# Optimization experiments

Measured on AMD Instinct MI355X. Metric: run time of the kernel, lower is better.

The kernel has to match this reference:

```python
import jax, jax.numpy as jnp
import numpy as np

T_STEPS, BATCH, DH, L = 256, 128, 512, 3  # L=3 is the only shape-consistent conv length (kernel=3, no pad)


def _conv3(x, W, b):
    # Conv1d(Dh->2, k=3) on a length-3 signal == full contraction over (Dh, 3)
    # x: (B, Dh, 3), W: (2, Dh, 3), b: (2,) -> (B, 2, 1)
    out = jnp.einsum('bdl,odl->bo', x, W) + b
    return out[:, :, None]


def setup_inputs() -> dict:
    key = jax.random.key(0)
    ks = jax.random.split(key, 5)
    inputs = jax.random.normal(ks[0], (T_STEPS, BATCH, DH, L), dtype=jnp.float32)
    h0 = jnp.zeros((BATCH, DH, L), jnp.float32)
    c0 = jnp.zeros((BATCH, DH, L), jnp.float32)
    scale = 1.0 / np.sqrt(DH * L).astype(np.float32)
    Wr = jax.random.normal(ks[1], (2, DH, L), jnp.float32) * scale  # recurrent_kernel (orthogonal-ish init)
    br = jnp.full((2,), 0.5, jnp.float32)                           # recurrent bias init 0.5
    Wc = jax.random.normal(ks[2], (2, DH, L), jnp.float32) * scale  # cell_memory_kernel
    bc = jnp.zeros((2,), jnp.float32)                               # cell_memory bias init 0
    Wi = jax.random.normal(ks[3], (2, DH, L), jnp.float32) * scale  # input_kernel
    bi = jax.random.normal(ks[4], (2,), jnp.float32) * scale
    return dict(inputs=inputs, h0=h0, c0=c0, Wr=Wr, br=br, Wc=Wc, bc=bc, Wi=Wi, bi=bi)


def reference(inputs, h0, c0, Wr, br, Wc, bc, Wi, bi):
    sig = jax.nn.sigmoid  # fun_gate

    def step(state, xt):
        h, c = state  # (B, Dh, 3) each
        cm = _conv3(c, Wc, bc)
        Cc, Ch = cm[:, 0:1], cm[:, 1:2]   # (B,1,1) each (chunk(2, dim=1))
        rm = _conv3(h, Wr, br)
        Hc, Hh = rm[:, 0:1], rm[:, 1:2]
        im = _conv3(xt, Wi, bi)
        Xc, Xh = im[:, 0:1], im[:, 1:2]
        gh = (1.0 - sig(Ch)) * Xh + (1.0 - sig(Hh)) * h   # broadcast (B,1,1)*(B,Dh,3)
        gc = (1.0 - sig(Hc)) * Xc + (1.0 - sig(Cc)) * c
        ht = jnp.tanh(gh)  # fun_main
        ct = jnp.tanh(gc)
        return (ht, ct), ht

    (hT, cT), outs = jax.lax.scan(step, (h0, c0), inputs)
    return outs, hT, cT
```

## Files before the change

### kernel.cpp

```cpp
#include <hip/hip_runtime.h>

#define T_STEPS 256
#define BATCH   128
#define FEAT    1536
#define NPAIRS  (T_STEPS * BATCH)

template <int CTRL, int RMASK>
__device__ __forceinline__ float dpp_add_step(float v) {
    int m = __builtin_amdgcn_update_dpp(0, __float_as_int(v), CTRL, RMASK, 0xF, true);
    return v + __int_as_float(m);
}

__device__ __forceinline__ float wave_reduce63(float v) {
    v = dpp_add_step<0x111, 0xF>(v);
    v = dpp_add_step<0x112, 0xF>(v);
    v = dpp_add_step<0x114, 0xF>(v);
    v = dpp_add_step<0x118, 0xF>(v);
    v = dpp_add_step<0x142, 0xA>(v);
    v = dpp_add_step<0x143, 0xC>(v);
    return v;
}

__device__ __forceinline__ float one_minus_sig(float x) {
    float e = __builtin_amdgcn_exp2f(x * 1.4426950408889634f);
    return __builtin_amdgcn_rcpf(1.0f + e);
}

__device__ __forceinline__ float tanh_fast(float x) {
    float e = __builtin_amdgcn_exp2f(x * 2.8853900817779268f);
    return fmaf(-2.0f, __builtin_amdgcn_rcpf(1.0f + e), 1.0f);
}

__device__ __forceinline__ void barrier_lds_only() {
    asm volatile("s_waitcnt lgkmcnt(0)\n\ts_barrier" ::: "memory");
}

__global__ __launch_bounds__(256) void scan_fused_kernel(
    const float* __restrict__ inputs,
    const float* __restrict__ h0,
    const float* __restrict__ c0,
    const float* __restrict__ Wr, const float* __restrict__ br,
    const float* __restrict__ Wc, const float* __restrict__ bc,
    const float* __restrict__ Wi, const float* __restrict__ bi,
    float* __restrict__ outs,
    float* __restrict__ hT,
    float* __restrict__ cT)
{
    const int b    = blockIdx.x;
    const int tid  = threadIdx.x;
    const int wid  = tid >> 6;
    const int lane = tid & 63;

    __shared__ float4 red4[2][4];
    __shared__ float2 red2[2][4];

    const float4 wr0_4 = ((const float4*)Wr)[tid];
    const float4 wr1_4 = ((const float4*)(Wr + FEAT))[tid];
    const float2 wr0_2 = ((const float2*)(Wr + 1024))[tid];
    const float2 wr1_2 = ((const float2*)(Wr + FEAT + 1024))[tid];
    const float4 wc0_4 = ((const float4*)Wc)[tid];
    const float4 wc1_4 = ((const float4*)(Wc + FEAT))[tid];
    const float2 wc0_2 = ((const float2*)(Wc + 1024))[tid];
    const float2 wc1_2 = ((const float2*)(Wc + FEAT + 1024))[tid];
    const float4 wi0_4 = ((const float4*)Wi)[tid];
    const float4 wi1_4 = ((const float4*)(Wi + FEAT))[tid];
    const float2 wi0_2 = ((const float2*)(Wi + 1024))[tid];
    const float2 wi1_2 = ((const float2*)(Wi + FEAT + 1024))[tid];
    const float br0 = br[0], br1 = br[1];
    const float bc0 = bc[0], bc1 = bc[1];
    const float bi0 = bi[0], bi1 = bi[1];

    const float* h0b = h0 + (size_t)b * FEAT;
    const float* c0b = c0 + (size_t)b * FEAT;
    float4 h4 = ((const float4*)h0b)[tid];
    float2 h2 = ((const float2*)(h0b + 1024))[tid];
    float4 c4 = ((const float4*)c0b)[tid];
    float2 c2 = ((const float2*)(c0b + 1024))[tid];

    const float*  xbase   = inputs + (size_t)b * FEAT;
    const size_t  XSTRIDE = (size_t)BATCH * FEAT;

    float4 xa4 = ((const float4*)xbase)[tid];
    float2 xa2 = ((const float2*)(xbase + 1024))[tid];
    float4 xb4 = ((const float4*)(xbase + XSTRIDE))[tid];
    float2 xb2 = ((const float2*)(xbase + XSTRIDE + 1024))[tid];

    float* op = outs + (size_t)b * FEAT;
    const size_t OSTRIDE = (size_t)BATCH * FEAT;

    auto step = [&](float4* buf4, float2* buf2, int t, float4& x4, float2& x2) {
        float pHc = h4.x * wr0_4.x + h4.y * wr0_4.y + h4.z * wr0_4.z + h4.w * wr0_4.w
                  + h2.x * wr0_2.x + h2.y * wr0_2.y;
        float pHh = h4.x * wr1_4.x + h4.y * wr1_4.y + h4.z * wr1_4.z + h4.w * wr1_4.w
                  + h2.x * wr1_2.x + h2.y * wr1_2.y;
        float pCc = c4.x * wc0_4.x + c4.y * wc0_4.y + c4.z * wc0_4.z + c4.w * wc0_4.w
                  + c2.x * wc0_2.x + c2.y * wc0_2.y;
        float pCh = c4.x * wc1_4.x + c4.y * wc1_4.y + c4.z * wc1_4.z + c4.w * wc1_4.w
                  + c2.x * wc1_2.x + c2.y * wc1_2.y;
        float pXc = x4.x * wi0_4.x + x4.y * wi0_4.y + x4.z * wi0_4.z + x4.w * wi0_4.w
                  + x2.x * wi0_2.x + x2.y * wi0_2.y;
        float pXh = x4.x * wi1_4.x + x4.y * wi1_4.y + x4.z * wi1_4.z + x4.w * wi1_4.w
                  + x2.x * wi1_2.x + x2.y * wi1_2.y;

        {
            const int tn = (t + 2 < T_STEPS) ? (t + 2) : (T_STEPS - 1);
            const float* xp = xbase + (size_t)tn * XSTRIDE;
            x4 = ((const float4*)xp)[tid];
            x2 = ((const float2*)(xp + 1024))[tid];
        }

        pHc = wave_reduce63(pHc);
        pHh = wave_reduce63(pHh);
        pCc = wave_reduce63(pCc);
        pCh = wave_reduce63(pCh);
        pXc = wave_reduce63(pXc);
        pXh = wave_reduce63(pXh);

        if (lane == 63) {
            buf4[wid] = make_float4(pHc, pHh, pCc, pCh);
            buf2[wid] = make_float2(pXc, pXh);
        }
        barrier_lds_only();
        const float4 r0 = buf4[0];
        const float4 r1 = buf4[1];
        const float4 r2 = buf4[2];
        const float4 r3 = buf4[3];
        const float2 s0 = buf2[0];
        const float2 s1 = buf2[1];
        const float2 s2 = buf2[2];
        const float2 s3 = buf2[3];
        const float Hc = r0.x + r1.x + r2.x + r3.x + br0;
        const float Hh = r0.y + r1.y + r2.y + r3.y + br1;
        const float Cc = r0.z + r1.z + r2.z + r3.z + bc0;
        const float Ch = r0.w + r1.w + r2.w + r3.w + bc1;
        const float Xc = s0.x + s1.x + s2.x + s3.x + bi0;
        const float Xh = s0.y + s1.y + s2.y + s3.y + bi1;

        const float Ah = one_minus_sig(Ch) * Xh;
        const float Sh = one_minus_sig(Hh);
        const float Ac = one_minus_sig(Hc) * Xc;
        const float Sc = one_minus_sig(Cc);

        h4.x = tanh_fast(fmaf(Sh, h4.x, Ah));
        h4.y = tanh_fast(fmaf(Sh, h4.y, Ah));
        h4.z = tanh_fast(fmaf(Sh, h4.z, Ah));
        h4.w = tanh_fast(fmaf(Sh, h4.w, Ah));
        h2.x = tanh_fast(fmaf(Sh, h2.x, Ah));
        h2.y = tanh_fast(fmaf(Sh, h2.y, Ah));

        c4.x = tanh_fast(fmaf(Sc, c4.x, Ac));
        c4.y = tanh_fast(fmaf(Sc, c4.y, Ac));
        c4.z = tanh_fast(fmaf(Sc, c4.z, Ac));
        c4.w = tanh_fast(fmaf(Sc, c4.w, Ac));
        c2.x = tanh_fast(fmaf(Sc, c2.x, Ac));
        c2.y = tanh_fast(fmaf(Sc, c2.y, Ac));

        ((float4*)op)[tid]          = h4;
        ((float2*)(op + 1024))[tid] = h2;
        op += OSTRIDE;
    };

#pragma unroll 1
    for (int t = 0; t < T_STEPS; t += 2) {
        step(red4[0], red2[0], t,     xa4, xa2);
        step(red4[1], red2[1], t + 1, xb4, xb2);
    }

    float* hp = hT + (size_t)b * FEAT;
    ((float4*)hp)[tid]          = h4;
    ((float2*)(hp + 1024))[tid] = h2;
    float* cp = cT + (size_t)b * FEAT;
    ((float4*)cp)[tid]          = c4;
    ((float2*)(cp + 1024))[tid] = c2;
}

extern "C" void kernel_launch(void* const* d_in, const int* in_sizes, int n_in,
                              void* d_out, int out_size, void* d_ws, size_t ws_size,
                              hipStream_t stream) {
    const float* inputs = (const float*)d_in[0];
    const float* h0     = (const float*)d_in[1];
    const float* c0     = (const float*)d_in[2];
    const float* Wr     = (const float*)d_in[3];
    const float* br     = (const float*)d_in[4];
    const float* Wc     = (const float*)d_in[5];
    const float* bc     = (const float*)d_in[6];
    const float* Wi     = (const float*)d_in[7];
    const float* bi     = (const float*)d_in[8];

    float* out  = (float*)d_out;
    float* outs = out;
    float* hT   = out + (size_t)NPAIRS * FEAT;
    float* cT   = hT + (size_t)BATCH * FEAT;

    scan_fused_kernel<<<BATCH, 256, 0, stream>>>(inputs, h0, c0, Wr, br,
                                                 Wc, bc, Wi, bi,
                                                 outs, hT, cT);
}
```

Measured before the change: 442.2 us.

## Software-pipeline input projection one step ahead, off the recurrent critical path

The input-kernel dot products and their wave reductions are moved after the barrier so each step computes the input projection for the next timestep while the recurrent reduction result is consumed. Results go through a 4-slot LDS ring, and input loads are prefetched four steps ahead in registers. This takes the input reduction off the per-step dependency chain between barriers, at the cost of more registers and a ring-index schedule that must line up exactly across the unrolled-by-4 loop.

```diff
diff --git a/kernel.cpp b/kernel.cpp
--- a/kernel.cpp
+++ b/kernel.cpp
@@ -52,7 +52,7 @@
     const int lane = tid & 63;
 
     __shared__ float4 red4[2][4];
-    __shared__ float2 red2[2][4];
+    __shared__ float2 XR[4][4];
 
     const float4 wr0_4 = ((const float4*)Wr)[tid];
     const float4 wr1_4 = ((const float4*)(Wr + FEAT))[tid];
@@ -80,15 +80,33 @@
     const float*  xbase   = inputs + (size_t)b * FEAT;
     const size_t  XSTRIDE = (size_t)BATCH * FEAT;
 
-    float4 xa4 = ((const float4*)xbase)[tid];
-    float2 xa2 = ((const float2*)(xbase + 1024))[tid];
-    float4 xb4 = ((const float4*)(xbase + XSTRIDE))[tid];
-    float2 xb2 = ((const float2*)(xbase + XSTRIDE + 1024))[tid];
+    {
+        const float4 x4 = ((const float4*)xbase)[tid];
+        const float2 x2 = ((const float2*)(xbase + 1024))[tid];
+        float pXc = x4.x * wi0_4.x + x4.y * wi0_4.y + x4.z * wi0_4.z + x4.w * wi0_4.w
+                  + x2.x * wi0_2.x + x2.y * wi0_2.y;
+        float pXh = x4.x * wi1_4.x + x4.y * wi1_4.y + x4.z * wi1_4.z + x4.w * wi1_4.w
+                  + x2.x * wi1_2.x + x2.y * wi1_2.y;
+        pXc = wave_reduce63(pXc);
+        pXh = wave_reduce63(pXh);
+        if (lane == 63) XR[3][wid] = make_float2(pXc, pXh);
+    }
+
+    float4 R1_4 = ((const float4*)(xbase + 1 * XSTRIDE))[tid];
+    float2 R1_2 = ((const float2*)(xbase + 1 * XSTRIDE + 1024))[tid];
+    float4 R2_4 = ((const float4*)(xbase + 2 * XSTRIDE))[tid];
+    float2 R2_2 = ((const float2*)(xbase + 2 * XSTRIDE + 1024))[tid];
+    float4 R3_4 = ((const float4*)(xbase + 3 * XSTRIDE))[tid];
+    float2 R3_2 = ((const float2*)(xbase + 3 * XSTRIDE + 1024))[tid];
+    float4 R0_4 = ((const float4*)(xbase + 4 * XSTRIDE))[tid];
+    float2 R0_2 = ((const float2*)(xbase + 4 * XSTRIDE + 1024))[tid];
 
     float* op = outs + (size_t)b * FEAT;
     const size_t OSTRIDE = (size_t)BATCH * FEAT;
 
-    auto step = [&](float4* buf4, float2* buf2, int t, float4& x4, float2& x2) {
+    __syncthreads();
+
+    auto step = [&](float4* buf, float4& rx4, float2& rx2, int t, int sw, int sr) {
         float pHc = h4.x * wr0_4.x + h4.y * wr0_4.y + h4.z * wr0_4.z + h4.w * wr0_4.w
                   + h2.x * wr0_2.x + h2.y * wr0_2.y;
         float pHh = h4.x * wr1_4.x + h4.y * wr1_4.y + h4.z * wr1_4.z + h4.w * wr1_4.w
@@ -97,38 +115,41 @@
                   + c2.x * wc0_2.x + c2.y * wc0_2.y;
         float pCh = c4.x * wc1_4.x + c4.y * wc1_4.y + c4.z * wc1_4.z + c4.w * wc1_4.w
                   + c2.x * wc1_2.x + c2.y * wc1_2.y;
-        float pXc = x4.x * wi0_4.x + x4.y * wi0_4.y + x4.z * wi0_4.z + x4.w * wi0_4.w
-                  + x2.x * wi0_2.x + x2.y * wi0_2.y;
-        float pXh = x4.x * wi1_4.x + x4.y * wi1_4.y + x4.z * wi1_4.z + x4.w * wi1_4.w
-                  + x2.x * wi1_2.x + x2.y * wi1_2.y;
-
-        {
-            const int tn = (t + 2 < T_STEPS) ? (t + 2) : (T_STEPS - 1);
-            const float* xp = xbase + (size_t)tn * XSTRIDE;
-            x4 = ((const float4*)xp)[tid];
-            x2 = ((const float2*)(xp + 1024))[tid];
-        }
 
         pHc = wave_reduce63(pHc);
         pHh = wave_reduce63(pHh);
         pCc = wave_reduce63(pCc);
         pCh = wave_reduce63(pCh);
+
+        if (lane == 63) {
+            buf[wid] = make_float4(pHc, pHh, pCc, pCh);
+        }
+        barrier_lds_only();
+        const float4 r0 = buf[0];
+        const float4 r1 = buf[1];
+        const float4 r2 = buf[2];
+        const float4 r3 = buf[3];
+        const float2 s0 = XR[sr][0];
+        const float2 s1 = XR[sr][1];
+        const float2 s2 = XR[sr][2];
+        const float2 s3 = XR[sr][3];
+
+        float pXc = rx4.x * wi0_4.x + rx4.y * wi0_4.y + rx4.z * wi0_4.z + rx4.w * wi0_4.w
+                  + rx2.x * wi0_2.x + rx2.y * wi0_2.y;
+        float pXh = rx4.x * wi1_4.x + rx4.y * wi1_4.y + rx4.z * wi1_4.z + rx4.w * wi1_4.w
+                  + rx2.x * wi1_2.x + rx2.y * wi1_2.y;
+        {
+            const int tn = (t + 5 < T_STEPS) ? (t + 5) : (T_STEPS - 1);
+            const float* xp = xbase + (size_t)tn * XSTRIDE;
+            rx4 = ((const float4*)xp)[tid];
+            rx2 = ((const float2*)(xp + 1024))[tid];
+        }
         pXc = wave_reduce63(pXc);
         pXh = wave_reduce63(pXh);
-
         if (lane == 63) {
-            buf4[wid] = make_float4(pHc, pHh, pCc, pCh);
-            buf2[wid] = make_float2(pXc, pXh);
+            XR[sw][wid] = make_float2(pXc, pXh);
         }
-        barrier_lds_only();
-        const float4 r0 = buf4[0];
-        const float4 r1 = buf4[1];
-        const float4 r2 = buf4[2];
-        const float4 r3 = buf4[3];
-        const float2 s0 = buf2[0];
-        const float2 s1 = buf2[1];
-        const float2 s2 = buf2[2];
-        const float2 s3 = buf2[3];
+
         const float Hc = r0.x + r1.x + r2.x + r3.x + br0;
         const float Hh = r0.y + r1.y + r2.y + r3.y + br1;
         const float Cc = r0.z + r1.z + r2.z + r3.z + bc0;
@@ -161,9 +182,11 @@
     };
 
 #pragma unroll 1
-    for (int t = 0; t < T_STEPS; t += 2) {
-        step(red4[0], red2[0], t,     xa4, xa2);
-        step(red4[1], red2[1], t + 1, xb4, xb2);
+    for (int t = 0; t < T_STEPS; t += 4) {
+        step(red4[0], R1_4, R1_2, t,     0, 3);
+        step(red4[1], R2_4, R2_2, t + 1, 1, 0);
+        step(red4[0], R3_4, R3_2, t + 2, 2, 1);
+        step(red4[1], R0_4, R0_2, t + 3, 3, 2);
     }
 
     float* hp = hT + (size_t)b * FEAT;
```

New measurement: 426.4 us. 3.6% less time.

## Split input projection into producer blocks feeding recurrent blocks via flags

Applied to the files above, without the earlier changes.

Launches twice as many blocks. The first half computes the input convolution for all timesteps of one batch row and publishes the two scalars per step to a workspace, with release-ordered progress counters. The second half runs the recurrence, spin-waiting on those counters and reading precomputed Xc/Xh four steps ahead, so the serial loop no longer streams inputs or does the input reductions. This takes input bandwidth and reduction work off the critical recurrent path. It relies on all 256 blocks being co-resident to avoid deadlock and adds a memset plus atomic polling.

```diff
diff --git a/kernel.cpp b/kernel.cpp
--- a/kernel.cpp
+++ b/kernel.cpp
@@ -35,7 +35,9 @@
     asm volatile("s_waitcnt lgkmcnt(0)\n\ts_barrier" ::: "memory");
 }
 
-__global__ __launch_bounds__(256) void scan_fused_kernel(
+union F2U { float2 f; unsigned long long u; };
+
+__global__ __launch_bounds__(256) void rg_cell_kernel(
     const float* __restrict__ inputs,
     const float* __restrict__ h0,
     const float* __restrict__ c0,
@@ -44,15 +46,68 @@
     const float* __restrict__ Wi, const float* __restrict__ bi,
     float* __restrict__ outs,
     float* __restrict__ hT,
-    float* __restrict__ cT)
+    float* __restrict__ cT,
+    float* __restrict__ Xws,
+    int*   __restrict__ prog)
 {
-    const int b    = blockIdx.x;
     const int tid  = threadIdx.x;
     const int wid  = tid >> 6;
     const int lane = tid & 63;
 
-    __shared__ float4 red4[2][4];
-    __shared__ float2 red2[2][4];
+    if (blockIdx.x < BATCH) {
+        const int b = blockIdx.x;
+
+        float4 wiA[6], wiB[6];
+#pragma unroll
+        for (int j = 0; j < 6; ++j) {
+            wiA[j] = *(const float4*)(Wi + j * 256 + lane * 4);
+            wiB[j] = *(const float4*)(Wi + FEAT + j * 256 + lane * 4);
+        }
+        const float bi0 = bi[0], bi1 = bi[1];
+
+        int* pr = prog + 4 * b + wid;
+        unsigned long long* Xb =
+            (unsigned long long*)((float2*)Xws + (size_t)b * T_STEPS);
+
+#pragma unroll 1
+        for (int k = 0; k < 64; ++k) {
+            const int t = (wid << 6) + k;
+            const float* xp = inputs + ((size_t)t * BATCH + b) * FEAT;
+            float4 xv[6];
+#pragma unroll
+            for (int j = 0; j < 6; ++j)
+                xv[j] = *(const float4*)(xp + j * 256 + lane * 4);
+
+            float a0 = 0.0f, a1 = 0.0f;
+#pragma unroll
+            for (int j = 0; j < 6; ++j) {
+                a0 = fmaf(xv[j].x, wiA[j].x, a0);
+                a0 = fmaf(xv[j].y, wiA[j].y, a0);
+                a0 = fmaf(xv[j].z, wiA[j].z, a0);
+                a0 = fmaf(xv[j].w, wiA[j].w, a0);
+                a1 = fmaf(xv[j].x, wiB[j].x, a1);
+                a1 = fmaf(xv[j].y, wiB[j].y, a1);
+                a1 = fmaf(xv[j].z, wiB[j].z, a1);
+                a1 = fmaf(xv[j].w, wiB[j].w, a1);
+            }
+            a0 = wave_reduce63(a0);
+            a1 = wave_reduce63(a1);
+            if (lane == 63) {
+                F2U q; q.f = make_float2(a0 + bi0, a1 + bi1);
+                __hip_atomic_store(Xb + t, q.u, __ATOMIC_RELAXED,
+                                   __HIP_MEMORY_SCOPE_AGENT);
+                if ((k & 3) == 3) {
+                    __hip_atomic_store(pr, k + 1, __ATOMIC_RELEASE,
+                                       __HIP_MEMORY_SCOPE_AGENT);
+                }
+            }
+        }
+        return;
+    }
+
+    const int b = blockIdx.x - BATCH;
+
+    __shared__ float4 red[2][4];
 
     const float4 wr0_4 = ((const float4*)Wr)[tid];
     const float4 wr1_4 = ((const float4*)(Wr + FEAT))[tid];
@@ -62,13 +117,8 @@
     const float4 wc1_4 = ((const float4*)(Wc + FEAT))[tid];
     const float2 wc0_2 = ((const float2*)(Wc + 1024))[tid];
     const float2 wc1_2 = ((const float2*)(Wc + FEAT + 1024))[tid];
-    const float4 wi0_4 = ((const float4*)Wi)[tid];
-    const float4 wi1_4 = ((const float4*)(Wi + FEAT))[tid];
-    const float2 wi0_2 = ((const float2*)(Wi + 1024))[tid];
-    const float2 wi1_2 = ((const float2*)(Wi + FEAT + 1024))[tid];
     const float br0 = br[0], br1 = br[1];
     const float bc0 = bc[0], bc1 = bc[1];
-    const float bi0 = bi[0], bi1 = bi[1];
 
     const float* h0b = h0 + (size_t)b * FEAT;
     const float* c0b = c0 + (size_t)b * FEAT;
@@ -77,18 +127,29 @@
     float4 c4 = ((const float4*)c0b)[tid];
     float2 c2 = ((const float2*)(c0b + 1024))[tid];
 
-    const float*  xbase   = inputs + (size_t)b * FEAT;
-    const size_t  XSTRIDE = (size_t)BATCH * FEAT;
-
-    float4 xa4 = ((const float4*)xbase)[tid];
-    float2 xa2 = ((const float2*)(xbase + 1024))[tid];
-    float4 xb4 = ((const float4*)(xbase + XSTRIDE))[tid];
-    float2 xb2 = ((const float2*)(xbase + XSTRIDE + 1024))[tid];
-
     float* op = outs + (size_t)b * FEAT;
     const size_t OSTRIDE = (size_t)BATCH * FEAT;
 
-    auto step = [&](float4* buf4, float2* buf2, int t, float4& x4, float2& x2) {
+    const unsigned long long* Xb =
+        (const unsigned long long*)((const float2*)Xws + (size_t)b * T_STEPS);
+    int* pr0 = prog + 4 * b;
+
+    int cur_chunk = 0;
+    int known = 0;
+
+    while (known < 4) {
+        known = __hip_atomic_load(pr0, __ATOMIC_ACQUIRE, __HIP_MEMORY_SCOPE_AGENT);
+    }
+    F2U q0, q1, q2, q3;
+    q0.u = __hip_atomic_load(Xb + 0, __ATOMIC_RELAXED, __HIP_MEMORY_SCOPE_AGENT);
+    q1.u = __hip_atomic_load(Xb + 1, __ATOMIC_RELAXED, __HIP_MEMORY_SCOPE_AGENT);
+    q2.u = __hip_atomic_load(Xb + 2, __ATOMIC_RELAXED, __HIP_MEMORY_SCOPE_AGENT);
+    q3.u = __hip_atomic_load(Xb + 3, __ATOMIC_RELAXED, __HIP_MEMORY_SCOPE_AGENT);
+    float2 xs0 = q0.f, xs1 = q1.f, xs2 = q2.f, xs3 = q3.f;
+
+    auto step = [&](float4* buf, int t, float2& xslot) {
+        const float2 Xv = xslot;
+
         float pHc = h4.x * wr0_4.x + h4.y * wr0_4.y + h4.z * wr0_4.z + h4.w * wr0_4.w
                   + h2.x * wr0_2.x + h2.y * wr0_2.y;
         float pHh = h4.x * wr1_4.x + h4.y * wr1_4.y + h4.z * wr1_4.z + h4.w * wr1_4.w
@@ -97,44 +158,44 @@
                   + c2.x * wc0_2.x + c2.y * wc0_2.y;
         float pCh = c4.x * wc1_4.x + c4.y * wc1_4.y + c4.z * wc1_4.z + c4.w * wc1_4.w
                   + c2.x * wc1_2.x + c2.y * wc1_2.y;
-        float pXc = x4.x * wi0_4.x + x4.y * wi0_4.y + x4.z * wi0_4.z + x4.w * wi0_4.w
-                  + x2.x * wi0_2.x + x2.y * wi0_2.y;
-        float pXh = x4.x * wi1_4.x + x4.y * wi1_4.y + x4.z * wi1_4.z + x4.w * wi1_4.w
-                  + x2.x * wi1_2.x + x2.y * wi1_2.y;
-
-        {
-            const int tn = (t + 2 < T_STEPS) ? (t + 2) : (T_STEPS - 1);
-            const float* xp = xbase + (size_t)tn * XSTRIDE;
-            x4 = ((const float4*)xp)[tid];
-            x2 = ((const float2*)(xp + 1024))[tid];
-        }
 
         pHc = wave_reduce63(pHc);
         pHh = wave_reduce63(pHh);
         pCc = wave_reduce63(pCc);
         pCh = wave_reduce63(pCh);
-        pXc = wave_reduce63(pXc);
-        pXh = wave_reduce63(pXh);
 
         if (lane == 63) {
-            buf4[wid] = make_float4(pHc, pHh, pCc, pCh);
-            buf2[wid] = make_float2(pXc, pXh);
+            buf[wid] = make_float4(pHc, pHh, pCc, pCh);
         }
         barrier_lds_only();
-        const float4 r0 = buf4[0];
-        const float4 r1 = buf4[1];
-        const float4 r2 = buf4[2];
-        const float4 r3 = buf4[3];
-        const float2 s0 = buf2[0];
-        const float2 s1 = buf2[1];
-        const float2 s2 = buf2[2];
-        const float2 s3 = buf2[3];
+        const float4 r0 = buf[0];
+        const float4 r1 = buf[1];
+        const float4 r2 = buf[2];
+        const float4 r3 = buf[3];
+
+        const int tq = t + 4;
+        if (tq < T_STEPS) {
+            const int cq = tq >> 6;
+            const int iq = tq & 63;
+            if (cq != cur_chunk) { cur_chunk = cq; known = 0; }
+            if (known <= iq) {
+                do {
+                    known = __hip_atomic_load(pr0 + cq, __ATOMIC_ACQUIRE,
+                                              __HIP_MEMORY_SCOPE_AGENT);
+                } while (known <= iq);
+            }
+            F2U qv;
+            qv.u = __hip_atomic_load(Xb + tq, __ATOMIC_RELAXED,
+                                     __HIP_MEMORY_SCOPE_AGENT);
+            xslot = qv.f;
+        }
+
         const float Hc = r0.x + r1.x + r2.x + r3.x + br0;
         const float Hh = r0.y + r1.y + r2.y + r3.y + br1;
         const float Cc = r0.z + r1.z + r2.z + r3.z + bc0;
         const float Ch = r0.w + r1.w + r2.w + r3.w + bc1;
-        const float Xc = s0.x + s1.x + s2.x + s3.x + bi0;
-        const float Xh = s0.y + s1.y + s2.y + s3.y + bi1;
+        const float Xc = Xv.x;
+        const float Xh = Xv.y;
 
         const float Ah = one_minus_sig(Ch) * Xh;
         const float Sh = one_minus_sig(Hh);
@@ -161,9 +222,11 @@
     };
 
 #pragma unroll 1
-    for (int t = 0; t < T_STEPS; t += 2) {
-        step(red4[0], red2[0], t,     xa4, xa2);
-        step(red4[1], red2[1], t + 1, xb4, xb2);
+    for (int t = 0; t < T_STEPS; t += 4) {
+        step(red[0], t,     xs0);
+        step(red[1], t + 1, xs1);
+        step(red[0], t + 2, xs2);
+        step(red[1], t + 3, xs3);
     }
 
     float* hp = hT + (size_t)b * FEAT;
@@ -192,7 +255,12 @@
     float* hT   = out + (size_t)NPAIRS * FEAT;
     float* cT   = hT + (size_t)BATCH * FEAT;
 
-    scan_fused_kernel<<<BATCH, 256, 0, stream>>>(inputs, h0, c0, Wr, br,
-                                                 Wc, bc, Wi, bi,
-                                                 outs, hT, cT);
-}
+    float* X    = (float*)d_ws;
+    int*   prog = (int*)((char*)d_ws + 256 * 1024);
+
+    hipMemsetAsync(prog, 0, BATCH * 4 * sizeof(int), stream);
+
+    rg_cell_kernel<<<2 * BATCH, 256, 0, stream>>>(inputs, h0, c0, Wr, br,
+                                                  Wc, bc, Wi, bi,
+                                                  outs, hT, cT, X, prog);
+}
```

Measured after the change: 881.6 us. 1.99x slower.
